# Kernel tuning notes

Hardware: AMD Instinct MI355X
Metric: run time of the kernel (lower is better)

Reference implementation:

```python
import jax, jax.numpy as jnp
import numpy as np

B, N, E, IDX = 4, 200000, 128, 2048


def setup_inputs() -> dict:
    key = jax.random.key(0)
    ks = jax.random.split(key, 6)
    x = jax.random.normal(ks[0], (B, N, E), dtype=jnp.float32)
    mask = jax.random.randint(ks[1], (B, N), 0, 2).astype(jnp.int32)
    index = jax.random.randint(ks[2], (B, N), 0, IDX).astype(jnp.int32)
    W = jax.random.normal(ks[3], (E, E), dtype=jnp.float32) * 0.05
    b = jax.random.normal(ks[4], (E,), dtype=jnp.float32) * 0.05
    context = jax.random.normal(ks[5], (E,), dtype=jnp.float32)
    return {"x": x, "W": W, "b": b, "context": context, "mask": mask, "index": index}


def _segment_attend(scores, idx, xb):
    # scores: [N], idx: [N] int, xb: [N, E]
    m = jax.ops.segment_max(scores, idx, num_segments=IDX)  # [IDX]
    m = jnp.where(jnp.isfinite(m), m, 0.0)  # empty segments -> -inf guard
    e = jnp.exp(scores - m[idx])
    ssum = jax.ops.segment_sum(e, idx, num_segments=IDX)  # [IDX]
    w = e / ssum[idx]  # segment softmax weights, [N]
    out = jax.ops.segment_sum(xb * w[:, None], idx, num_segments=IDX)  # [IDX, E]
    return out, w


def reference(x, W, b, context, mask, index):
    norm = jnp.sqrt(jnp.asarray(E, dtype=x.dtype))
    hidden = jnp.tanh(jnp.einsum('bne,fe->bnf', x, W) + b)  # Linear(E,E) + tanh
    importance = jnp.einsum('bne,e->bn', hidden, context) / norm
    importance = jnp.where(mask == 0, jnp.asarray(-1e9, dtype=x.dtype), importance)
    out, attn = jax.vmap(_segment_attend)(importance, index, x)
    return out, attn
```

## Files before the change

kernel.cpp:

```cpp
#include <hip/hip_runtime.h>
#include <hip/hip_bf16.h>
#include <math.h>

#define B_    4
#define N_    200000
#define E_    128
#define IDX_  2048
#define TT    (B_*N_)
#define INV_NORM 0.08838834764831845f
#define CAPB  128
#define WPAD  136

typedef __attribute__((ext_vector_type(8))) short bf16x8;
typedef __attribute__((ext_vector_type(4))) float f32x4;

__device__ __forceinline__ unsigned short f2bf(float f) {
    unsigned int u = __float_as_uint(f);
    unsigned int r = (u + 0x7fffu + ((u >> 16) & 1u)) >> 16;
    return (unsigned short)r;
}

__global__ __launch_bounds__(256) void build_kernel(
    const int* __restrict__ index, const int* __restrict__ mask,
    int* __restrict__ cursor, int* __restrict__ toklist,
    int* __restrict__ posmap, float* __restrict__ attn)
{
    int tok = blockIdx.x * blockDim.x + threadIdx.x;
    if (tok >= TT) return;
    int pos = -1;
    if (mask[tok]) {
        int key  = (tok / N_) * IDX_ + index[tok];
        int slot = atomicAdd(&cursor[key], 1);
        if (slot < CAPB) {
            pos = key * CAPB + slot;
            toklist[pos] = tok;
        }
    } else {
        attn[tok] = 0.f;
    }
    posmap[tok] = pos;
}

__global__ __launch_bounds__(256) void score_kernel(
    const float* __restrict__ x, const float* __restrict__ W,
    const float* __restrict__ bias, const float* __restrict__ ctx,
    const int* __restrict__ mask, const int* __restrict__ posmap,
    float* __restrict__ pscore)
{
    __shared__ unsigned short Wb[E_ * WPAD];

    const int tid = threadIdx.x;

    for (int i = tid; i < E_ * E_ / 4; i += 256) {
        int f = i >> 5, kb = (i & 31) * 4;
        float4 v = ((const float4*)W)[i];
        ushort4 o;
        o.x = f2bf(v.x); o.y = f2bf(v.y); o.z = f2bf(v.z); o.w = f2bf(v.w);
        *(ushort4*)&Wb[f * WPAD + kb] = o;
    }
    __syncthreads();

    const int lane = tid & 63;
    const int col  = lane & 15;
    const int q    = lane >> 4;
    const int wave = tid >> 6;

    float ctx_r[8], bias2[8], csum = 0.f;
#pragma unroll
    for (int n = 0; n < 8; n++) {
        ctx_r[n] = ctx[n * 16 + col];
        bias2[n] = 2.f * bias[n * 16 + col];
        csum += ctx_r[n];
    }
    const float csum_n = csum * INV_NORM;

    bf16x8 Bf[8][4];
#pragma unroll
    for (int n = 0; n < 8; n++)
#pragma unroll
        for (int kt = 0; kt < 4; kt++)
            Bf[n][kt] = *(const bf16x8*)&Wb[(n * 16 + col) * WPAD + kt * 32 + q * 8];

    for (long base0 = (long)blockIdx.x * 64; base0 < TT; base0 += (long)gridDim.x * 64) {
        const long tbase = base0 + wave * 16;
        const float* xrow = x + (tbase + col) * (long)E_;

        const int mrow = mask[tbase + col];

        bf16x8 Af[4];
#pragma unroll
        for (int kt = 0; kt < 4; kt++)
            Af[kt] = (bf16x8){0, 0, 0, 0, 0, 0, 0, 0};
        if (mrow) {
#pragma unroll
            for (int kt = 0; kt < 4; kt++) {
                float4 u = ((const float4*)xrow)[kt * 8 + q * 2];
                float4 v = ((const float4*)xrow)[kt * 8 + q * 2 + 1];
                union { bf16x8 vec; __hip_bfloat162 h[4]; } a;
                a.h[0] = __float22bfloat162_rn(make_float2(u.x, u.y));
                a.h[1] = __float22bfloat162_rn(make_float2(u.z, u.w));
                a.h[2] = __float22bfloat162_rn(make_float2(v.x, v.y));
                a.h[3] = __float22bfloat162_rn(make_float2(v.z, v.w));
                Af[kt] = a.vec;
            }
        }

        f32x4 acc[8];
#pragma unroll
        for (int n = 0; n < 8; n++) acc[n] = (f32x4){0.f, 0.f, 0.f, 0.f};

#pragma unroll
        for (int kt = 0; kt < 4; kt++)
#pragma unroll
            for (int n = 0; n < 8; n++)
                acc[n] = __builtin_amdgcn_mfma_f32_16x16x32_bf16(Af[kt], Bf[n][kt], acc[n], 0, 0, 0);

        float pr[4];
#pragma unroll
        for (int r = 0; r < 4; r++) {
            float psum = 0.f;
#pragma unroll
            for (int n = 0; n < 8; n++) {
                float t = fmaf(acc[n][r], 2.f, bias2[n]);
                float rc = __builtin_amdgcn_rcpf(1.f + __expf(t));
                psum = fmaf(ctx_r[n], rc, psum);
            }
            float p = fmaf(-2.f * INV_NORM, psum, csum_n);
#pragma unroll
            for (int o = 1; o < 16; o <<= 1) p += __shfl_xor(p, o);
            pr[r] = p;
        }
        if (col == 0) {
            int4 pm = ((const int4*)(posmap + tbase))[q];
            if (pm.x >= 0) pscore[pm.x] = pr[0];
            if (pm.y >= 0) pscore[pm.y] = pr[1];
            if (pm.z >= 0) pscore[pm.z] = pr[2];
            if (pm.w >= 0) pscore[pm.w] = pr[3];
        }
    }
}

__global__ __launch_bounds__(256) void attend_kernel(
    const float* __restrict__ x, const int* __restrict__ cursor,
    const int* __restrict__ toklist, const float* __restrict__ pscore,
    float* __restrict__ attn , float* __restrict__ out)
{
    const int wave = threadIdx.x >> 6;
    const int lane = threadIdx.x & 63;
    const int key  = blockIdx.x * 4 + wave;
    const int cnt  = min(cursor[key], CAPB);
    const int base = key * CAPB;
    const float2* __restrict__ x2 = (const float2*)x;
    float2* out2 = (float2*)(out + (size_t)key * E_);

    __shared__ int2 pair[4][CAPB];

    if (cnt == 0) { out2[lane] = make_float2(0.f, 0.f); return; }

    int   tk[2];
    float sc[2], ev[2];
    float m = -INFINITY;
#pragma unroll
    for (int u = 0; u < 2; u++) {
        int j = lane + u * 64;
        if (j < cnt) {
            tk[u] = toklist[base + j];
            sc[u] = pscore[base + j];
            m = fmaxf(m, sc[u]);
        }
    }
#pragma unroll
    for (int o = 32; o; o >>= 1) m = fmaxf(m, __shfl_xor(m, o));

    float sum = 0.f;
#pragma unroll
    for (int u = 0; u < 2; u++) {
        int j = lane + u * 64;
        if (j < cnt) { ev[u] = __expf(sc[u] - m); sum += ev[u]; }
    }
#pragma unroll
    for (int o = 32; o; o >>= 1) sum += __shfl_xor(sum, o);
    const float inv = 1.f / sum;

#pragma unroll
    for (int u = 0; u < 2; u++) {
        int j = lane + u * 64;
        if (j < cnt) {
            float w = ev[u] * inv;
            attn[tk[u]] = w;
            pair[wave][j] = make_int2(tk[u], __float_as_int(w));
        }
    }

    float2 acc = make_float2(0.f, 0.f);
    int j = 0;
    for (; j + 3 < cnt; j += 4) {
        int2 p0 = pair[wave][j];
        int2 p1 = pair[wave][j + 1];
        int2 p2 = pair[wave][j + 2];
        int2 p3 = pair[wave][j + 3];
        float2 a0 = x2[(size_t)p0.x * 64 + lane];
        float2 a1 = x2[(size_t)p1.x * 64 + lane];
        float2 a2 = x2[(size_t)p2.x * 64 + lane];
        float2 a3 = x2[(size_t)p3.x * 64 + lane];
        float w0 = __int_as_float(p0.y), w1 = __int_as_float(p1.y);
        float w2 = __int_as_float(p2.y), w3 = __int_as_float(p3.y);
        acc.x = fmaf(w0, a0.x, acc.x); acc.y = fmaf(w0, a0.y, acc.y);
        acc.x = fmaf(w1, a1.x, acc.x); acc.y = fmaf(w1, a1.y, acc.y);
        acc.x = fmaf(w2, a2.x, acc.x); acc.y = fmaf(w2, a2.y, acc.y);
        acc.x = fmaf(w3, a3.x, acc.x); acc.y = fmaf(w3, a3.y, acc.y);
    }
    for (; j < cnt; j++) {
        int2  p = pair[wave][j];
        float2 a = x2[(size_t)p.x * 64 + lane];
        float w = __int_as_float(p.y);
        acc.x = fmaf(w, a.x, acc.x); acc.y = fmaf(w, a.y, acc.y);
    }
    out2[lane] = acc;
}

extern "C" void kernel_launch(void* const* d_in, const int* in_sizes, int n_in,
                              void* d_out, int out_size, void* d_ws, size_t ws_size,
                              hipStream_t stream)
{
    const float* x    = (const float*)d_in[0];
    const float* W    = (const float*)d_in[1];
    const float* bias = (const float*)d_in[2];
    const float* ctx  = (const float*)d_in[3];
    const int*   mask = (const int*)d_in[4];
    const int*   index= (const int*)d_in[5];

    float* out  = (float*)d_out;
    float* attn = out + (size_t)B_ * IDX_ * E_;

    int*   cursor  = (int*)d_ws;
    int*   toklist = cursor  + B_ * IDX_;
    int*   posmap  = toklist + B_ * IDX_ * CAPB;
    float* pscore  = (float*)(posmap + TT);

    hipMemsetAsync(cursor, 0, B_ * IDX_ * sizeof(int), stream);
    build_kernel  <<<(TT + 255) / 256, 256, 0, stream>>>(index, mask, cursor, toklist, posmap, attn);
    score_kernel  <<<2048, 256, 0, stream>>>(x, W, bias, ctx, mask, posmap, pscore);
    attend_kernel <<<B_ * IDX_ / 4, 256, 0, stream>>>(x, cursor, toklist, pscore, attn, out);
}
```

Before: 609.0 us.

## Fuse bucket build into score kernel and store token/score pairs together

Removes the separate build kernel. Segment bucketing via atomicAdd now happens inside the score kernel's epilogue, which writes (token, score) pairs into a single per-segment list. This drops a launch plus the posmap and toklist traffic, and lets the attend kernel read one int2 per entry instead of two arrays. In exchange, the atomics are issued serially by one lane per 4 rows inside the compute-bound kernel, which may add latency there.

After: 632.8 us. +3.9%, slower.

```diff
diff --git a/kernel.cpp b/kernel.cpp
--- a/kernel.cpp
+++ b/kernel.cpp
@@ -20,32 +20,12 @@
     return (unsigned short)r;
 }
 
-__global__ __launch_bounds__(256) void build_kernel(
-    const int* __restrict__ index, const int* __restrict__ mask,
-    int* __restrict__ cursor, int* __restrict__ toklist,
-    int* __restrict__ posmap, float* __restrict__ attn)
-{
-    int tok = blockIdx.x * blockDim.x + threadIdx.x;
-    if (tok >= TT) return;
-    int pos = -1;
-    if (mask[tok]) {
-        int key  = (tok / N_) * IDX_ + index[tok];
-        int slot = atomicAdd(&cursor[key], 1);
-        if (slot < CAPB) {
-            pos = key * CAPB + slot;
-            toklist[pos] = tok;
-        }
-    } else {
-        attn[tok] = 0.f;
-    }
-    posmap[tok] = pos;
-}
-
 __global__ __launch_bounds__(256) void score_kernel(
     const float* __restrict__ x, const float* __restrict__ W,
     const float* __restrict__ bias, const float* __restrict__ ctx,
-    const int* __restrict__ mask, const int* __restrict__ posmap,
-    float* __restrict__ pscore)
+    const int* __restrict__ mask, const int* __restrict__ index,
+    int* __restrict__ cursor, int2* __restrict__ plist,
+    float* __restrict__ attn)
 {
     __shared__ unsigned short Wb[E_ * WPAD];
 
@@ -131,18 +111,31 @@
             pr[r] = p;
         }
         if (col == 0) {
-            int4 pm = ((const int4*)(posmap + tbase))[q];
-            if (pm.x >= 0) pscore[pm.x] = pr[0];
-            if (pm.y >= 0) pscore[pm.y] = pr[1];
-            if (pm.z >= 0) pscore[pm.z] = pr[2];
-            if (pm.w >= 0) pscore[pm.w] = pr[3];
+            int4 mv = ((const int4*)(mask + tbase))[q];
+            int4 iv = ((const int4*)(index + tbase))[q];
+            const int  bofs = (int)(tbase / N_) * IDX_;
+            const long t0   = tbase + q * 4;
+#pragma unroll
+            for (int r = 0; r < 4; r++) {
+                int mr = (r == 0) ? mv.x : (r == 1) ? mv.y : (r == 2) ? mv.z : mv.w;
+                int ir = (r == 0) ? iv.x : (r == 1) ? iv.y : (r == 2) ? iv.z : iv.w;
+                int tok = (int)(t0 + r);
+                if (mr) {
+                    int key  = bofs + ir;
+                    int slot = atomicAdd(&cursor[key], 1);
+                    if (slot < CAPB)
+                        plist[key * CAPB + slot] = make_int2(tok, __float_as_int(pr[r]));
+                } else {
+                    attn[tok] = 0.f;
+                }
+            }
         }
     }
 }
 
 __global__ __launch_bounds__(256) void attend_kernel(
     const float* __restrict__ x, const int* __restrict__ cursor,
-    const int* __restrict__ toklist, const float* __restrict__ pscore,
+    const int2* __restrict__ plist,
     float* __restrict__ attn , float* __restrict__ out)
 {
     const int wave = threadIdx.x >> 6;
@@ -164,8 +157,9 @@
     for (int u = 0; u < 2; u++) {
         int j = lane + u * 64;
         if (j < cnt) {
-            tk[u] = toklist[base + j];
-            sc[u] = pscore[base + j];
+            int2 p = plist[base + j];
+            tk[u] = p.x;
+            sc[u] = __int_as_float(p.y);
             m = fmaxf(m, sc[u]);
         }
     }
@@ -233,13 +227,10 @@
     float* out  = (float*)d_out;
     float* attn = out + (size_t)B_ * IDX_ * E_;
 
-    int*   cursor  = (int*)d_ws;
-    int*   toklist = cursor  + B_ * IDX_;
-    int*   posmap  = toklist + B_ * IDX_ * CAPB;
-    float* pscore  = (float*)(posmap + TT);
+    int*  cursor = (int*)d_ws;
+    int2* plist  = (int2*)(cursor + B_ * IDX_);
 
     hipMemsetAsync(cursor, 0, B_ * IDX_ * sizeof(int), stream);
-    build_kernel  <<<(TT + 255) / 256, 256, 0, stream>>>(index, mask, cursor, toklist, posmap, attn);
-    score_kernel  <<<2048, 256, 0, stream>>>(x, W, bias, ctx, mask, posmap, pscore);
-    attend_kernel <<<B_ * IDX_ / 4, 256, 0, stream>>>(x, cursor, toklist, pscore, attn, out);
-}
+    score_kernel  <<<2048, 256, 0, stream>>>(x, W, bias, ctx, mask, index, cursor, plist, attn);
+    attend_kernel <<<B_ * IDX_ / 4, 256, 0, stream>>>(x, cursor, plist, attn, out);
+}
```
